# Optimization experiments

Measured on AMD Instinct MI355X. Metric: run time of the kernel, lower is better.

## Reference

```python
import jax, jax.numpy as jnp
import numpy as np

L, B = 256, 512
K, IN, STATE, OBS = 128, 64, 128, 128


def _preprocess(x, w1, b1, w2, b2):
    # PreProcess: two Linear+ReLU layers mapping raw dim -> k
    t = jax.nn.relu(x @ w1.T + b1)
    return jax.nn.relu(t @ w2.T + b2)


def _dblock_relu(x, w1, b1, w2, b2, wmu, bmu, wls, bls):
    # DBlock (TD-VAE style) with ReLU in place of tanh:
    # t = relu(fc1(x)) * sigmoid(fc2(x)); mu = fc_mu(t); logsigma = fc_logsigma(t)
    t = jax.nn.relu(x @ w1.T + b1) * jax.nn.sigmoid(x @ w2.T + b2)
    return t @ wmu.T + bmu, t @ wls.T + bls


def setup_inputs() -> dict:
    key = jax.random.key(0)
    ks = jax.random.split(key, 24)
    rn = lambda i, shape, s=1.0: jax.random.normal(ks[i], shape, dtype=jnp.float32) * s
    W = 0.05  # small weight scale for numerical stability
    return {
        "external_input_seq": rn(0, (L, B, IN)),
        "observations_seq": rn(1, (L, B, OBS)),
        "eps": rn(2, (L, B, STATE)),
        "u_w1": rn(3, (K, IN), W), "u_b1": jnp.zeros((K,), jnp.float32),
        "u_w2": rn(4, (K, K), W), "u_b2": jnp.zeros((K,), jnp.float32),
        "x_w1": rn(5, (K, OBS), W), "x_b1": jnp.zeros((K,), jnp.float32),
        "x_w2": rn(6, (K, K), W), "x_b2": jnp.zeros((K,), jnp.float32),
        "post_w1": rn(7, (2 * K, 2 * K), W), "post_b1": jnp.zeros((2 * K,), jnp.float32),
        "post_w2": rn(8, (2 * K, 2 * K), W), "post_b2": jnp.zeros((2 * K,), jnp.float32),
        "post_wmu": rn(9, (STATE, 2 * K), W), "post_bmu": jnp.zeros((STATE,), jnp.float32),
        "post_wls": rn(10, (STATE, 2 * K), W), "post_bls": jnp.zeros((STATE,), jnp.float32),
        "gru_wih": rn(11, (3 * K, K), W), "gru_whh": rn(12, (3 * K, K), W),
        "gru_bih": jnp.zeros((3 * K,), jnp.float32), "gru_bhh": jnp.zeros((3 * K,), jnp.float32),
    }


def reference(external_input_seq, observations_seq, eps,
              u_w1, u_b1, u_w2, u_b2,
              x_w1, x_b1, x_w2, x_b2,
              post_w1, post_b1, post_w2, post_b2,
              post_wmu, post_bmu, post_wls, post_bls,
              gru_wih, gru_whh, gru_bih, gru_bhh):
    # _forward_posterior of VAERNN (num_layers=1 GRU)
    u_embed = _preprocess(external_input_seq, u_w1, u_b1, u_w2, u_b2)  # (L,B,K)
    x_embed = _preprocess(observations_seq, x_w1, x_b1, x_w2, x_b2)    # (L,B,K)

    # Precompute input-side GRU gates for all timesteps (one big GEMM)
    x_gates = u_embed @ gru_wih.T + gru_bih  # (L,B,3K)

    h0 = jnp.zeros((external_input_seq.shape[1], K), dtype=external_input_seq.dtype)

    def step(h, xg):
        hg = h @ gru_whh.T + gru_bhh
        xr, xz, xn = jnp.split(xg, 3, axis=-1)
        hr, hz, hn_ = jnp.split(hg, 3, axis=-1)
        r = jax.nn.sigmoid(xr + hr)
        z = jax.nn.sigmoid(xz + hz)
        n = jnp.tanh(xn + r * hn_)
        h_new = (1.0 - z) * n + z * h
        return h_new, h  # emit PRE-update hidden (matches h_seq[:-1])

    hn_final, h_seq = jax.lax.scan(step, h0, x_gates)  # h_seq: (L,B,K)

    # Posterior q(z_t | o_t, h_{t-1}) -- fully parallel over time since z_t
    # never feeds back into the recurrence in this model.
    post_in = jnp.concatenate([x_embed, h_seq], axis=-1)  # (L,B,2K)
    state_mu, state_logsigma = _dblock_relu(
        post_in, post_w1, post_b1, post_w2, post_b2,
        post_wmu, post_bmu, post_wls, post_bls)
    # reparameterized sample from N(mu, diag(exp(logsigma)^2))
    sampled_state = state_mu + jnp.exp(state_logsigma) * eps

    return state_mu, state_logsigma, sampled_state, h_seq, x_embed
```

## Files before the change

kernel.cpp:

```cpp
#include <hip/hip_runtime.h>


typedef __attribute__((ext_vector_type(8))) short bf16x8;
typedef __attribute__((ext_vector_type(4))) short bf16x4;
typedef __attribute__((ext_vector_type(4))) float f32x4;

#define LB 131072

__device__ __forceinline__ short f2b(float f) {
  union { float f; unsigned u; } v; v.f = f;
  unsigned r = (v.u + 0x7FFFu + ((v.u >> 16) & 1u)) >> 16;
  return (short)r;
}
__device__ __forceinline__ float u2f(unsigned u) {
  union { unsigned u; float f; } v; v.u = u << 16; return v.f;
}
__device__ __forceinline__ float rcpf(float x) { return __builtin_amdgcn_rcpf(x); }
__device__ __forceinline__ float exp2f_(float x) { return __builtin_amdgcn_exp2f(x); }
__device__ __forceinline__ float sigm(float x) { return rcpf(1.f + exp2f_(-1.44269504f * x)); }

#define LGKM_BAR()                                          \
  asm volatile("s_waitcnt lgkmcnt(0)" ::: "memory");        \
  __builtin_amdgcn_s_barrier();                             \
  __builtin_amdgcn_sched_barrier(0);

__global__ __launch_bounds__(256) void k_cvt(
    const float* __restrict__ s0, const float* __restrict__ s1,
    const float* __restrict__ s2, const float* __restrict__ s3,
    const float* __restrict__ s4, const float* __restrict__ s5,
    const float* __restrict__ s6, const float* __restrict__ s7,
    const float* __restrict__ s8, const float* __restrict__ s9,
    short* __restrict__ dst)
{
  int i = blockIdx.x * 256 + threadIdx.x;
  if (i >= 352256) return;
  const float* src; int off;
  if      (i <   8192) { src = s0; off = i; }
  else if (i <  24576) { src = s1; off = i - 8192; }
  else if (i <  40960) { src = s2; off = i - 24576; }
  else if (i <  57344) { src = s3; off = i - 40960; }
  else if (i < 106496) { src = s4; off = i - 57344; }
  else if (i < 155648) { src = s5; off = i - 106496; }
  else if (i < 221184) { src = s6; off = i - 155648; }
  else if (i < 286720) { src = s7; off = i - 221184; }
  else if (i < 319488) { src = s8; off = i - 286720; }
  else                 { src = s9; off = i - 319488; }
  dst[i] = f2b(src[off]);
}

#define UT 8
__global__ __launch_bounds__(512) void k_upath(
    const float* __restrict__ x, const short* __restrict__ w1, const float* __restrict__ b1,
    const short* __restrict__ w2, const float* __restrict__ b2,
    const short* __restrict__ wih, const float* __restrict__ bih,
    const float* __restrict__ bhh,
    short* __restrict__ gates)
{
  __shared__ short Xb[32][72];
  __shared__ short Tb[32][136];
  __shared__ short Gb[32][392];
  const int tid = threadIdx.x, w = tid >> 6, l = tid & 63;
  const int lr = l & 15, lg = l >> 4;
  const int n1 = w * 16 + lr;

  bf16x8 wf1[2], wf2[4], wfg[3][4];
  #pragma unroll
  for (int kt = 0; kt < 2; ++kt)
    wf1[kt] = *reinterpret_cast<const bf16x8*>(w1 + (size_t)n1 * 64 + kt * 32 + lg * 8);
  #pragma unroll
  for (int kt = 0; kt < 4; ++kt)
    wf2[kt] = *reinterpret_cast<const bf16x8*>(w2 + (size_t)n1 * 128 + kt * 32 + lg * 8);
  float bgv[3];
  #pragma unroll
  for (int j = 0; j < 3; ++j) {
    const int cg = w * 48 + j * 16 + lr;
    bgv[j] = bih[cg] + (cg < 256 ? bhh[cg] : 0.f);
    #pragma unroll
    for (int kt = 0; kt < 4; ++kt)
      wfg[j][kt] = *reinterpret_cast<const bf16x8*>(wih + (size_t)cg * 128 + kt * 32 + lg * 8);
  }
  const float b1v = b1[n1], b2v = b2[n1];
  const int srow = tid >> 4, scol4 = (tid & 15) * 4, gcol = (tid & 15) * 24;

  for (int it = 0; it < UT; ++it) {
    const size_t m0 = ((size_t)blockIdx.x * UT + it) * 32;

    {
      float4 v = *reinterpret_cast<const float4*>(x + (m0 + srow) * 64 + scol4);
      bf16x4 p; p[0] = f2b(v.x); p[1] = f2b(v.y); p[2] = f2b(v.z); p[3] = f2b(v.w);
      *reinterpret_cast<bf16x4*>(&Xb[srow][scol4]) = p;
    }
    LGKM_BAR();

    f32x4 a1c[2] = {(f32x4){0.f,0.f,0.f,0.f}, (f32x4){0.f,0.f,0.f,0.f}};
    #pragma unroll
    for (int kt = 0; kt < 2; ++kt) {
      #pragma unroll
      for (int mt = 0; mt < 2; ++mt) {
        bf16x8 af = *reinterpret_cast<const bf16x8*>(&Xb[mt * 16 + lr][kt * 32 + lg * 8]);
        a1c[mt] = __builtin_amdgcn_mfma_f32_16x16x32_bf16(af, wf1[kt], a1c[mt], 0, 0, 0);
      }
    }
    #pragma unroll
    for (int mt = 0; mt < 2; ++mt)
      #pragma unroll
      for (int r = 0; r < 4; ++r) {
        float v = a1c[mt][r] + b1v;
        Tb[mt * 16 + lg * 4 + r][n1] = f2b(v > 0.f ? v : 0.f);
      }
    LGKM_BAR();

    f32x4 a2c[2] = {(f32x4){0.f,0.f,0.f,0.f}, (f32x4){0.f,0.f,0.f,0.f}};
    #pragma unroll
    for (int kt = 0; kt < 4; ++kt) {
      #pragma unroll
      for (int mt = 0; mt < 2; ++mt) {
        bf16x8 af = *reinterpret_cast<const bf16x8*>(&Tb[mt * 16 + lr][kt * 32 + lg * 8]);
        a2c[mt] = __builtin_amdgcn_mfma_f32_16x16x32_bf16(af, wf2[kt], a2c[mt], 0, 0, 0);
      }
    }
    #pragma unroll
    for (int mt = 0; mt < 2; ++mt)
      #pragma unroll
      for (int r = 0; r < 4; ++r) {
        float v = a2c[mt][r] + b2v;
        Gb[mt * 16 + lg * 4 + r][n1] = f2b(v > 0.f ? v : 0.f);
      }
    LGKM_BAR();

    bf16x8 ag[2][4];
    #pragma unroll
    for (int mt = 0; mt < 2; ++mt)
      #pragma unroll
      for (int kt = 0; kt < 4; ++kt)
        ag[mt][kt] = *reinterpret_cast<const bf16x8*>(&Gb[mt * 16 + lr][kt * 32 + lg * 8]);
    LGKM_BAR();

    #pragma unroll
    for (int j = 0; j < 3; ++j) {
      #pragma unroll
      for (int mt = 0; mt < 2; ++mt) {
        f32x4 c = {0.f, 0.f, 0.f, 0.f};
        #pragma unroll
        for (int kt = 0; kt < 4; ++kt)
          c = __builtin_amdgcn_mfma_f32_16x16x32_bf16(ag[mt][kt], wfg[j][kt], c, 0, 0, 0);
        #pragma unroll
        for (int r = 0; r < 4; ++r)
          Gb[mt * 16 + lg * 4 + r][w * 48 + j * 16 + lr] = f2b(c[r] + bgv[j]);
      }
    }
    LGKM_BAR();

    #pragma unroll
    for (int k = 0; k < 3; ++k) {
      bf16x8 vv = *reinterpret_cast<const bf16x8*>(&Gb[srow][gcol + k * 8]);
      *reinterpret_cast<bf16x8*>(gates + (m0 + srow) * 384 + gcol + k * 8) = vv;
    }
  }
}

__global__ __launch_bounds__(512) void k_grux(
    const short* __restrict__ gates, const short* __restrict__ whh,
    const float* __restrict__ bhh, float* __restrict__ hseq,
    const float* __restrict__ obs, const short* __restrict__ xw1,
    const float* __restrict__ xb1, const short* __restrict__ xw2,
    const float* __restrict__ xb2, float* __restrict__ xe)
{
  __shared__ short smem_[8 * 32 * 136];
  const int tid = threadIdx.x, w = tid >> 6, l = tid & 63;
  const int lr = l & 15, lg = l >> 4;

  if (blockIdx.x < 64) {
    short (*hb)[16][136] = reinterpret_cast<short (*)[16][136]>(smem_);
    const int m0 = blockIdx.x * 8;
    const int c = w * 16 + lr;

    bf16x8 bfr[3][4];
    #pragma unroll
    for (int g = 0; g < 3; ++g)
      #pragma unroll
      for (int kt = 0; kt < 4; ++kt)
        bfr[g][kt] = *reinterpret_cast<const bf16x8*>(whh + (size_t)(g * 128 + c) * 128 + kt * 32 + lg * 8);
    const float bbn = bhh[256 + c];

    for (int i = tid; i < 2 * 16 * 136; i += 512) smem_[i] = 0;

    const int mk0 = (lg & 1) * 4 + (lg >> 1) * 2;
    const int mk1 = mk0 + 1;
    const size_t gr0 = m0 + mk0, gr1 = m0 + mk1;

    float hold[2] = {0.f, 0.f};

    unsigned gA[3][2], gB[3][2];
    #pragma unroll
    for (int g = 0; g < 3; ++g) {
      gA[g][0] = (unsigned short)gates[gr0 * 384 + g * 128 + c];
      gA[g][1] = (unsigned short)gates[gr1 * 384 + g * 128 + c];
      gB[g][0] = (unsigned short)gates[(512 + gr0) * 384 + g * 128 + c];
      gB[g][1] = (unsigned short)gates[(512 + gr1) * 384 + g * 128 + c];
    }

    __syncthreads();

#define GRU_STEP(T, GC, BR, BW)                                                \
  {                                                                            \
    const int t_ = (T);                                                        \
    bf16x8 a_[4];                                                              \
    _Pragma("unroll")                                                          \
    for (int kt = 0; kt < 4; ++kt)                                             \
      a_[kt] = *reinterpret_cast<const bf16x8*>(&hb[BR][lr][kt * 32 + lg * 8]);\
    float e_[3][2];                                                            \
    _Pragma("unroll")                                                          \
    for (int g = 0; g < 3; ++g) {                                              \
      f32x4 cc = {0.f, 0.f, 0.f, 0.f};                                         \
      _Pragma("unroll")                                                        \
      for (int kt = 0; kt < 4; ++kt)                                           \
        cc = __builtin_amdgcn_mfma_f32_16x16x32_bf16(a_[kt], bfr[g][kt], cc, 0, 0, 0); \
      unsigned u0 = __float_as_uint(cc[0]), u2 = __float_as_uint(cc[2]);       \
      unsigned u1 = __float_as_uint(cc[1]), u3 = __float_as_uint(cc[3]);       \
      asm volatile("v_permlane32_swap_b32 %0, %1" : "+v"(u0), "+v"(u2));       \
      asm volatile("v_permlane32_swap_b32 %0, %1" : "+v"(u1), "+v"(u3));       \
      e_[g][0] = __uint_as_float(u0);                                          \
      e_[g][1] = __uint_as_float(u1);                                          \
    }                                                                          \
    _Pragma("unroll")                                                          \
    for (int k = 0; k < 2; ++k) {                                              \
      const int mk = k ? mk1 : mk0;                                            \
      const size_t grk = k ? gr1 : gr0;                                        \
      float rr = sigm(u2f(GC[0][k]) + e_[0][k]);                               \
      float zz = sigm(u2f(GC[1][k]) + e_[1][k]);                               \
      float tt = u2f(GC[2][k]) + (e_[2][k] + bbn) * rr;                        \
      float nn = 1.f - 2.f * rcpf(1.f + exp2f_(2.88539008f * tt));             \
      float ho = hold[k];                                                      \
      float hnew = nn + zz * (ho - nn);                                        \
      hseq[((size_t)t_ * 512 + grk) * 128 + c] = ho;                           \
      hold[k] = hnew;                                                          \
      hb[BW][mk][c] = f2b(hnew);                                               \
    }                                                                          \
    const int tp_ = (t_ + 2) & 255;                                            \
    _Pragma("unroll")                                                          \
    for (int g = 0; g < 3; ++g) {                                              \
      GC[g][0] = (unsigned short)gates[((size_t)tp_ * 512 + gr0) * 384 + g * 128 + c]; \
      GC[g][1] = (unsigned short)gates[((size_t)tp_ * 512 + gr1) * 384 + g * 128 + c]; \
    }                                                                          \
    asm volatile("s_waitcnt lgkmcnt(0)" ::: "memory");                         \
    __builtin_amdgcn_s_barrier();                                              \
    __builtin_amdgcn_sched_barrier(0);                                         \
  }

    for (int tt = 0; tt < 128; ++tt) {
      GRU_STEP(2 * tt,     gA, 0, 1)
      GRU_STEP(2 * tt + 1, gB, 1, 0)
    }
#undef GRU_STEP
  } else {
    const int m0 = (blockIdx.x - 64) * 256 + w * 32;
    short (* __restrict__ B)[136] = reinterpret_cast<short (*)[136]>(&smem_[w * 32 * 136]);

    #pragma unroll
    for (int it = 0; it < 16; ++it) {
      int idx = (it * 64 + l) * 4;
      int row = idx >> 7, col = idx & 127;
      float4 v = *reinterpret_cast<const float4*>(obs + (size_t)(m0 + row) * 128 + col);
      bf16x4 p; p[0] = f2b(v.x); p[1] = f2b(v.y); p[2] = f2b(v.z); p[3] = f2b(v.w);
      *reinterpret_cast<bf16x4*>(&B[row][col]) = p;
    }

    f32x4 acc[2][8];
    bf16x8 a1f[2][4];
    #pragma unroll
    for (int mt = 0; mt < 2; ++mt)
      #pragma unroll
      for (int kt = 0; kt < 4; ++kt)
        a1f[mt][kt] = *reinterpret_cast<const bf16x8*>(&B[mt * 16 + lr][kt * 32 + lg * 8]);
    #pragma unroll
    for (int nt = 0; nt < 8; ++nt)
      #pragma unroll
      for (int mt = 0; mt < 2; ++mt) {
        f32x4 c = {0.f, 0.f, 0.f, 0.f};
        #pragma unroll
        for (int kt = 0; kt < 4; ++kt) {
          bf16x8 bv = *reinterpret_cast<const bf16x8*>(xw1 + (size_t)(nt * 16 + lr) * 128 + kt * 32 + lg * 8);
          c = __builtin_amdgcn_mfma_f32_16x16x32_bf16(a1f[mt][kt], bv, c, 0, 0, 0);
        }
        acc[mt][nt] = c;
      }
    #pragma unroll
    for (int nt = 0; nt < 8; ++nt) {
      float bb = xb1[nt * 16 + lr];
      #pragma unroll
      for (int mt = 0; mt < 2; ++mt)
        #pragma unroll
        for (int r = 0; r < 4; ++r) {
          float v = acc[mt][nt][r] + bb;
          B[mt * 16 + lg * 4 + r][nt * 16 + lr] = f2b(v > 0.f ? v : 0.f);
        }
    }

    bf16x8 a2f[2][4];
    #pragma unroll
    for (int mt = 0; mt < 2; ++mt)
      #pragma unroll
      for (int kt = 0; kt < 4; ++kt)
        a2f[mt][kt] = *reinterpret_cast<const bf16x8*>(&B[mt * 16 + lr][kt * 32 + lg * 8]);
    #pragma unroll
    for (int nt = 0; nt < 8; ++nt) {
      float bb = xb2[nt * 16 + lr];
      #pragma unroll
      for (int mt = 0; mt < 2; ++mt) {
        f32x4 c = {0.f, 0.f, 0.f, 0.f};
        #pragma unroll
        for (int kt = 0; kt < 4; ++kt) {
          bf16x8 bv = *reinterpret_cast<const bf16x8*>(xw2 + (size_t)(nt * 16 + lr) * 128 + kt * 32 + lg * 8);
          c = __builtin_amdgcn_mfma_f32_16x16x32_bf16(a2f[mt][kt], bv, c, 0, 0, 0);
        }
        #pragma unroll
        for (int r = 0; r < 4; ++r) {
          float v = c[r] + bb;
          xe[(size_t)(m0 + mt * 16 + lg * 4 + r) * 128 + nt * 16 + lr] = (v > 0.f ? v : 0.f);
        }
      }
    }
  }
}

#define PT 8
__global__ __launch_bounds__(512) void k_post(
    const float* __restrict__ xe, const float* __restrict__ hs, const float* __restrict__ eps,
    const short* __restrict__ pw1, const float* __restrict__ pb1,
    const short* __restrict__ pw2, const float* __restrict__ pb2,
    const short* __restrict__ pwmu, const float* __restrict__ pbmu,
    const short* __restrict__ pwls, const float* __restrict__ pbls,
    float* __restrict__ mu, float* __restrict__ ls, float* __restrict__ samp)
{
  __shared__ short Ab[32][264];
  const int tid = threadIdx.x, w = tid >> 6, l = tid & 63;
  const int lr = l & 15, lg = l >> 4;
  const int srow = tid >> 4, scol = (tid & 15) * 8;
  const int n2 = w * 16 + lr;

  bf16x8 wf1[2][8];
  float bb1[2], bb2[2];
  #pragma unroll
  for (int j = 0; j < 2; ++j) {
    const int n = w * 32 + j * 16 + lr;
    bb1[j] = pb1[n]; bb2[j] = pb2[n];
    #pragma unroll
    for (int kt = 0; kt < 8; ++kt)
      wf1[j][kt] = *reinterpret_cast<const bf16x8*>(pw1 + (size_t)n * 256 + kt * 32 + lg * 8);
  }
  const float bbm = pbmu[n2], bbl = pbls[n2];

  for (int it = 0; it < PT; ++it) {
    const size_t m0 = ((size_t)blockIdx.x * PT + it) * 32;

    unsigned long long a2 = (unsigned long long)pw2;
    unsigned long long am_ = (unsigned long long)pwmu;
    unsigned long long al_ = (unsigned long long)pwls;
    asm volatile("" : "+s"(a2), "+s"(am_), "+s"(al_));
    const short* pw2v = (const short*)a2;
    const short* pwmv = (const short*)am_;
    const short* pwlv = (const short*)al_;

    float ev[2][4];
    #pragma unroll
    for (int mt = 0; mt < 2; ++mt)
      #pragma unroll
      for (int r = 0; r < 4; ++r)
        ev[mt][r] = eps[(m0 + mt * 16 + lg * 4 + r) * 128 + n2];

    {
      const float* px = xe + (m0 + srow) * 128 + scol;
      float4 v0 = *reinterpret_cast<const float4*>(px);
      float4 v1 = *reinterpret_cast<const float4*>(px + 4);
      bf16x8 pk;
      pk[0] = f2b(v0.x); pk[1] = f2b(v0.y); pk[2] = f2b(v0.z); pk[3] = f2b(v0.w);
      pk[4] = f2b(v1.x); pk[5] = f2b(v1.y); pk[6] = f2b(v1.z); pk[7] = f2b(v1.w);
      *reinterpret_cast<bf16x8*>(&Ab[srow][scol]) = pk;
      const float* ph = hs + (m0 + srow) * 128 + scol;
      float4 h0 = *reinterpret_cast<const float4*>(ph);
      float4 h1 = *reinterpret_cast<const float4*>(ph + 4);
      bf16x8 qk;
      qk[0] = f2b(h0.x); qk[1] = f2b(h0.y); qk[2] = f2b(h0.z); qk[3] = f2b(h0.w);
      qk[4] = f2b(h1.x); qk[5] = f2b(h1.y); qk[6] = f2b(h1.z); qk[7] = f2b(h1.w);
      *reinterpret_cast<bf16x8*>(&Ab[srow][128 + scol]) = qk;
    }
    LGKM_BAR();

    bf16x8 wf2[2][8];
    #pragma unroll
    for (int j = 0; j < 2; ++j) {
      const int n = w * 32 + j * 16 + lr;
      #pragma unroll
      for (int kt = 0; kt < 8; ++kt)
        wf2[j][kt] = *reinterpret_cast<const bf16x8*>(pw2v + (size_t)n * 256 + kt * 32 + lg * 8);
    }
    f32x4 ac1[2][2], ac2[2][2];
    #pragma unroll
    for (int j = 0; j < 2; ++j)
      #pragma unroll
      for (int mt = 0; mt < 2; ++mt) { ac1[j][mt] = (f32x4){0.f,0.f,0.f,0.f}; ac2[j][mt] = (f32x4){0.f,0.f,0.f,0.f}; }
    #pragma unroll
    for (int kt = 0; kt < 8; ++kt) {
      bf16x8 af[2];
      #pragma unroll
      for (int mt = 0; mt < 2; ++mt)
        af[mt] = *reinterpret_cast<const bf16x8*>(&Ab[mt * 16 + lr][kt * 32 + lg * 8]);
      #pragma unroll
      for (int j = 0; j < 2; ++j)
        #pragma unroll
        for (int mt = 0; mt < 2; ++mt) {
          ac1[j][mt] = __builtin_amdgcn_mfma_f32_16x16x32_bf16(af[mt], wf1[j][kt], ac1[j][mt], 0, 0, 0);
          ac2[j][mt] = __builtin_amdgcn_mfma_f32_16x16x32_bf16(af[mt], wf2[j][kt], ac2[j][mt], 0, 0, 0);
        }
    }

    bf16x8 wm[8], wl[8];
    #pragma unroll
    for (int kt = 0; kt < 8; ++kt) {
      wm[kt] = *reinterpret_cast<const bf16x8*>(pwmv + (size_t)n2 * 256 + kt * 32 + lg * 8);
      wl[kt] = *reinterpret_cast<const bf16x8*>(pwlv + (size_t)n2 * 256 + kt * 32 + lg * 8);
    }
    LGKM_BAR();

    #pragma unroll
    for (int j = 0; j < 2; ++j)
      #pragma unroll
      for (int mt = 0; mt < 2; ++mt)
        #pragma unroll
        for (int r = 0; r < 4; ++r) {
          float t1 = ac1[j][mt][r] + bb1[j]; t1 = t1 > 0.f ? t1 : 0.f;
          float t2 = sigm(ac2[j][mt][r] + bb2[j]);
          Ab[mt * 16 + lg * 4 + r][w * 32 + j * 16 + lr] = f2b(t1 * t2);
        }
    LGKM_BAR();

    f32x4 amc[2], alc[2];
    #pragma unroll
    for (int mt = 0; mt < 2; ++mt) { amc[mt] = (f32x4){0.f,0.f,0.f,0.f}; alc[mt] = (f32x4){0.f,0.f,0.f,0.f}; }
    #pragma unroll
    for (int kt = 0; kt < 8; ++kt) {
      bf16x8 at[2];
      #pragma unroll
      for (int mt = 0; mt < 2; ++mt)
        at[mt] = *reinterpret_cast<const bf16x8*>(&Ab[mt * 16 + lr][kt * 32 + lg * 8]);
      #pragma unroll
      for (int mt = 0; mt < 2; ++mt) {
        amc[mt] = __builtin_amdgcn_mfma_f32_16x16x32_bf16(at[mt], wm[kt], amc[mt], 0, 0, 0);
        alc[mt] = __builtin_amdgcn_mfma_f32_16x16x32_bf16(at[mt], wl[kt], alc[mt], 0, 0, 0);
      }
    }
    #pragma unroll
    for (int mt = 0; mt < 2; ++mt)
      #pragma unroll
      for (int r = 0; r < 4; ++r) {
        size_t off = (m0 + mt * 16 + lg * 4 + r) * 128 + n2;
        float m_ = amc[mt][r] + bbm;
        float l_ = alc[mt][r] + bbl;
        mu[off] = m_;
        ls[off] = l_;
        samp[off] = m_ + exp2f_(1.44269504f * l_) * ev[mt][r];
      }
    LGKM_BAR();
  }
}

extern "C" void kernel_launch(void* const* d_in, const int* in_sizes, int n_in,
                              void* d_out, int out_size, void* d_ws, size_t ws_size,
                              hipStream_t stream) {
  const float* ext   = (const float*)d_in[0];
  const float* obs   = (const float*)d_in[1];
  const float* eps   = (const float*)d_in[2];
  const float* u_w1  = (const float*)d_in[3];
  const float* u_b1  = (const float*)d_in[4];
  const float* u_w2  = (const float*)d_in[5];
  const float* u_b2  = (const float*)d_in[6];
  const float* x_w1  = (const float*)d_in[7];
  const float* x_b1  = (const float*)d_in[8];
  const float* x_w2  = (const float*)d_in[9];
  const float* x_b2  = (const float*)d_in[10];
  const float* pw1   = (const float*)d_in[11];
  const float* pb1   = (const float*)d_in[12];
  const float* pw2   = (const float*)d_in[13];
  const float* pb2   = (const float*)d_in[14];
  const float* pwmu  = (const float*)d_in[15];
  const float* pbmu  = (const float*)d_in[16];
  const float* pwls  = (const float*)d_in[17];
  const float* pbls  = (const float*)d_in[18];
  const float* g_wih = (const float*)d_in[19];
  const float* g_whh = (const float*)d_in[20];
  const float* g_bih = (const float*)d_in[21];
  const float* g_bhh = (const float*)d_in[22];

  float* out = (float*)d_out;
  float* o_mu = out;
  float* o_ls = out + 16777216;
  float* o_sp = out + 33554432;
  float* o_hs = out + 50331648;
  float* o_xe = out + 67108864;
  short* gates = (short*)out;

  short* wb = (short*)d_ws;
  short* c_uw1  = wb + 0;
  short* c_uw2  = wb + 8192;
  short* c_xw1  = wb + 24576;
  short* c_xw2  = wb + 40960;
  short* c_wih  = wb + 57344;
  short* c_whh  = wb + 106496;
  short* c_pw1  = wb + 155648;
  short* c_pw2  = wb + 221184;
  short* c_pwmu = wb + 286720;
  short* c_pwls = wb + 319488;

  k_cvt<<<1376, 256, 0, stream>>>(u_w1, u_w2, x_w1, x_w2, g_wih, g_whh,
                                  pw1, pw2, pwmu, pwls, wb);
  k_upath<<<512, 512, 0, stream>>>(ext, c_uw1, u_b1, c_uw2, u_b2, c_wih, g_bih, g_bhh, gates);
  k_grux<<<576, 512, 0, stream>>>(gates, c_whh, g_bhh, o_hs,
                                  obs, c_xw1, x_b1, c_xw2, x_b2, o_xe);
  k_post<<<512, 512, 0, stream>>>(o_xe, o_hs, eps, c_pw1, pb1, c_pw2, pb2,
                                  c_pwmu, pbmu, c_pwls, pbls, o_mu, o_ls, o_sp);
}
```

Measured before the change: 421.2 us.

## Split GRU recurrence across 128 blocks with four batch rows each

The sequential GRU scan now runs on 128 blocks instead of 64, each handling 4 batch rows rather than 8. Each lane then handles a single row's gate math per step, using an extra permlane16 swap to route the MFMA outputs. This shortens the per-step serial elementwise and store work on the latency-bound recurrence path. In exchange, the MFMA tiles carry more padding rows and the recurrence occupies more CUs, leaving fewer for the concurrent x-embedding blocks.

```diff
diff --git a/kernel.cpp b/kernel.cpp
--- a/kernel.cpp
+++ b/kernel.cpp
@@ -170,10 +170,12 @@
   const int tid = threadIdx.x, w = tid >> 6, l = tid & 63;
   const int lr = l & 15, lg = l >> 4;
 
-  if (blockIdx.x < 64) {
+  if (blockIdx.x < 128) {
     short (*hb)[16][136] = reinterpret_cast<short (*)[16][136]>(smem_);
-    const int m0 = blockIdx.x * 8;
+    const int m0 = blockIdx.x * 4;
     const int c = w * 16 + lr;
+    const int row = lg;
+    const size_t gr = m0 + row;
 
     bf16x8 bfr[3][4];
     #pragma unroll
@@ -185,19 +187,13 @@
 
     for (int i = tid; i < 2 * 16 * 136; i += 512) smem_[i] = 0;
 
-    const int mk0 = (lg & 1) * 4 + (lg >> 1) * 2;
-    const int mk1 = mk0 + 1;
-    const size_t gr0 = m0 + mk0, gr1 = m0 + mk1;
-
-    float hold[2] = {0.f, 0.f};
-
-    unsigned gA[3][2], gB[3][2];
+    float hold = 0.f;
+
+    unsigned gA[3], gB[3];
     #pragma unroll
     for (int g = 0; g < 3; ++g) {
-      gA[g][0] = (unsigned short)gates[gr0 * 384 + g * 128 + c];
-      gA[g][1] = (unsigned short)gates[gr1 * 384 + g * 128 + c];
-      gB[g][0] = (unsigned short)gates[(512 + gr0) * 384 + g * 128 + c];
-      gB[g][1] = (unsigned short)gates[(512 + gr1) * 384 + g * 128 + c];
+      gA[g] = (unsigned short)gates[gr * 384 + g * 128 + c];
+      gB[g] = (unsigned short)gates[(512 + gr) * 384 + g * 128 + c];
     }
 
     __syncthreads();
@@ -209,40 +205,32 @@
     _Pragma("unroll")                                                          \
     for (int kt = 0; kt < 4; ++kt)                                             \
       a_[kt] = *reinterpret_cast<const bf16x8*>(&hb[BR][lr][kt * 32 + lg * 8]);\
-    float e_[3][2];                                                            \
+    float e_[3];                                                               \
     _Pragma("unroll")                                                          \
     for (int g = 0; g < 3; ++g) {                                              \
       f32x4 cc = {0.f, 0.f, 0.f, 0.f};                                         \
       _Pragma("unroll")                                                        \
       for (int kt = 0; kt < 4; ++kt)                                           \
         cc = __builtin_amdgcn_mfma_f32_16x16x32_bf16(a_[kt], bfr[g][kt], cc, 0, 0, 0); \
-      unsigned u0 = __float_as_uint(cc[0]), u2 = __float_as_uint(cc[2]);       \
-      unsigned u1 = __float_as_uint(cc[1]), u3 = __float_as_uint(cc[3]);       \
-      asm volatile("v_permlane32_swap_b32 %0, %1" : "+v"(u0), "+v"(u2));       \
-      asm volatile("v_permlane32_swap_b32 %0, %1" : "+v"(u1), "+v"(u3));       \
-      e_[g][0] = __uint_as_float(u0);                                          \
-      e_[g][1] = __uint_as_float(u1);                                          \
+    unsigned u0 = __float_as_uint(cc[0]), u2 = __float_as_uint(cc[2]);         \
+    unsigned u1 = __float_as_uint(cc[1]), u3 = __float_as_uint(cc[3]);         \
+    asm volatile("v_permlane32_swap_b32 %0, %1" : "+v"(u0), "+v"(u2));         \
+    asm volatile("v_permlane32_swap_b32 %0, %1" : "+v"(u1), "+v"(u3));         \
+    asm volatile("v_permlane16_swap_b32 %0, %1" : "+v"(u0), "+v"(u1));         \
+      e_[g] = __uint_as_float(u0);                                             \
     }                                                                          \
-    _Pragma("unroll")                                                          \
-    for (int k = 0; k < 2; ++k) {                                              \
-      const int mk = k ? mk1 : mk0;                                            \
-      const size_t grk = k ? gr1 : gr0;                                        \
-      float rr = sigm(u2f(GC[0][k]) + e_[0][k]);                               \
-      float zz = sigm(u2f(GC[1][k]) + e_[1][k]);                               \
-      float tt = u2f(GC[2][k]) + (e_[2][k] + bbn) * rr;                        \
-      float nn = 1.f - 2.f * rcpf(1.f + exp2f_(2.88539008f * tt));             \
-      float ho = hold[k];                                                      \
-      float hnew = nn + zz * (ho - nn);                                        \
-      hseq[((size_t)t_ * 512 + grk) * 128 + c] = ho;                           \
-      hold[k] = hnew;                                                          \
-      hb[BW][mk][c] = f2b(hnew);                                               \
-    }                                                                          \
+    float rr = sigm(u2f(GC[0]) + e_[0]);                                       \
+    float zz = sigm(u2f(GC[1]) + e_[1]);                                       \
+    float tt = u2f(GC[2]) + (e_[2] + bbn) * rr;                                \
+    float nn = 1.f - 2.f * rcpf(1.f + exp2f_(2.88539008f * tt));               \
+    float hnew = nn + zz * (hold - nn);                                        \
+    hseq[((size_t)t_ * 512 + gr) * 128 + c] = hold;                            \
+    hold = hnew;                                                               \
+    hb[BW][row][c] = f2b(hnew);                                                \
     const int tp_ = (t_ + 2) & 255;                                            \
     _Pragma("unroll")                                                          \
-    for (int g = 0; g < 3; ++g) {                                              \
-      GC[g][0] = (unsigned short)gates[((size_t)tp_ * 512 + gr0) * 384 + g * 128 + c]; \
-      GC[g][1] = (unsigned short)gates[((size_t)tp_ * 512 + gr1) * 384 + g * 128 + c]; \
-    }                                                                          \
+    for (int g = 0; g < 3; ++g)                                                \
+      GC[g] = (unsigned short)gates[((size_t)tp_ * 512 + gr) * 384 + g * 128 + c]; \
     asm volatile("s_waitcnt lgkmcnt(0)" ::: "memory");                         \
     __builtin_amdgcn_s_barrier();                                              \
     __builtin_amdgcn_sched_barrier(0);                                         \
@@ -254,7 +242,7 @@
     }
 #undef GRU_STEP
   } else {
-    const int m0 = (blockIdx.x - 64) * 256 + w * 32;
+    const int m0 = (blockIdx.x - 128) * 256 + w * 32;
     short (* __restrict__ B)[136] = reinterpret_cast<short (*)[136]>(&smem_[w * 32 * 136]);
 
     #pragma unroll
@@ -515,7 +503,7 @@
   k_cvt<<<1376, 256, 0, stream>>>(u_w1, u_w2, x_w1, x_w2, g_wih, g_whh,
                                   pw1, pw2, pwmu, pwls, wb);
   k_upath<<<512, 512, 0, stream>>>(ext, c_uw1, u_b1, c_uw2, u_b2, c_wih, g_bih, g_bhh, gates);
-  k_grux<<<576, 512, 0, stream>>>(gates, c_whh, g_bhh, o_hs,
+  k_grux<<<640, 512, 0, stream>>>(gates, c_whh, g_bhh, o_hs,
                                   obs, c_xw1, x_b1, c_xw2, x_b2, o_xe);
   k_post<<<512, 512, 0, stream>>>(o_xe, o_hs, eps, c_pw1, pb1, c_pw2, pb2,
                                   c_pwmu, pbmu, c_pwls, pbls, o_mu, o_ls, o_sp);
```

Result: faster. 412.4 us (-2.1%).
